# Kernel tuning notes

Measured on AMD Instinct MI355X. Metric: run time of the kernel, lower is better.

Reference implementation:

```python
import jax, jax.numpy as jnp
import numpy as np
from jax import lax

WIN = 7            # skimage default win_size
K1, K2 = 0.01, 0.03
DATA_RANGE = 1.0


def _uniform_filter_valid(x):
    # (skimage uses reflect-padded uniform_filter then crops pad=3, which equals
    #  a valid windowed mean.)
    c, h, w = x.shape
    x4 = x[:, None]                                   # (C,1,H,W)
    kh = jnp.full((1, 1, WIN, 1), 1.0 / WIN, x.dtype)
    kw = jnp.full((1, 1, 1, WIN), 1.0 / WIN, x.dtype)
    dn = ('NCHW', 'OIHW', 'NCHW')
    x4 = lax.conv_general_dilated(x4, kh, (1, 1), 'VALID', dimension_numbers=dn)
    x4 = lax.conv_general_dilated(x4, kw, (1, 1), 'VALID', dimension_numbers=dn)
    return x4[:, 0]


def setup_inputs() -> dict:
    key = jax.random.key(0)
    k1, k2 = jax.random.split(key)
    shape = (32, 3, 512, 512)
    return {
        'input_tensor': jax.random.uniform(k1, shape, dtype=jnp.float32),
        'target': jax.random.uniform(k2, shape, dtype=jnp.float32),
    }


def reference(input_tensor, target):
    h, w = input_tensor.shape[-2:]
    x = input_tensor.reshape(-1, h, w).astype(jnp.float32)
    y = target.reshape(-1, h, w).astype(jnp.float32)

    C1 = (K1 * DATA_RANGE) ** 2
    C2 = (K2 * DATA_RANGE) ** 2
    NP = WIN * WIN
    cov_norm = NP / (NP - 1.0)  # sample covariance (skimage default)

    ux = _uniform_filter_valid(x)
    uy = _uniform_filter_valid(y)
    uxx = _uniform_filter_valid(x * x)
    uyy = _uniform_filter_valid(y * y)
    uxy = _uniform_filter_valid(x * y)

    vx = cov_norm * (uxx - ux * ux)
    vy = cov_norm * (uyy - uy * uy)
    vxy = cov_norm * (uxy - ux * uy)

    S = ((2.0 * ux * uy + C1) * (2.0 * vxy + C2)) / (
        (ux * ux + uy * uy + C1) * (vx + vy + C2))
    # mean over cropped spatial map per channel, then over channels == global mean
    return jnp.mean(S)
```

## Files before the change

### kernel.cpp

```cpp
#include <hip/hip_runtime.h>


namespace {
constexpr int W       = 512;
constexpr int HH      = 512;
constexpr int NIMG    = 96;
constexpr int OW      = 506;
constexpr int RSTRIP  = 11;
constexpr int NSTRIP  = 46;
constexpr int WAVES   = NIMG * NSTRIP;
constexpr int BLOCKS  = WAVES / 4;
constexpr int NXCD    = 8;
constexpr int CPX     = BLOCKS / NXCD;
constexpr float C1s   = 0.2401f;
constexpr float C2s   = 2.1609f;
constexpr float COVN  = 49.0f / 48.0f;
constexpr double NPIX = 96.0 * 506.0 * 506.0;
}

__device__ __forceinline__ void load8(const float* __restrict__ p, float (&v)[8])
{
    float4 a = *(const float4*)(p);
    float4 b = *(const float4*)(p + 4);
    v[0] = a.x; v[1] = a.y; v[2] = a.z; v[3] = a.w;
    v[4] = b.x; v[5] = b.y; v[6] = b.z; v[7] = b.w;
}

__device__ __forceinline__ void vadd(float (&V)[5][8], const float (&x)[8], const float (&y)[8])
{
#pragma unroll
    for (int k = 0; k < 8; k++) {
        V[0][k] += x[k];
        V[1][k] += y[k];
        V[2][k] = fmaf(x[k], x[k], V[2][k]);
        V[3][k] = fmaf(y[k], y[k], V[3][k]);
        V[4][k] = fmaf(x[k], y[k], V[4][k]);
    }
}

__device__ __forceinline__ void vsub(float (&V)[5][8], const float (&x)[8], const float (&y)[8])
{
#pragma unroll
    for (int k = 0; k < 8; k++) {
        V[0][k] -= x[k];
        V[1][k] -= y[k];
        V[2][k] = fmaf(-x[k], x[k], V[2][k]);
        V[3][k] = fmaf(-y[k], y[k], V[3][k]);
        V[4][k] = fmaf(-x[k], y[k], V[4][k]);
    }
}

__device__ __forceinline__ void hssim(const float (&V)[5][8], float& sacc, int c0)
{
    float Hh[5][8];
#pragma unroll
    for (int q = 0; q < 5; q++) {
        float P[8];
        P[0] = V[q][0];
#pragma unroll
        for (int k = 1; k < 8; k++) P[k] = P[k - 1] + V[q][k];
        const float Pn0 = __shfl_down(P[0], 1);
        const float Pn1 = __shfl_down(P[1], 1);
        const float Pn2 = __shfl_down(P[2], 1);
        const float Pn3 = __shfl_down(P[3], 1);
        const float Pn4 = __shfl_down(P[4], 1);
        const float Pn5 = __shfl_down(P[5], 1);
        const float T = P[7];
        Hh[q][0] = P[6];
        Hh[q][1] = T - P[0];
        Hh[q][2] = (T - P[1]) + Pn0;
        Hh[q][3] = (T - P[2]) + Pn1;
        Hh[q][4] = (T - P[3]) + Pn2;
        Hh[q][5] = (T - P[4]) + Pn3;
        Hh[q][6] = (T - P[5]) + Pn4;
        Hh[q][7] = (T - P[6]) + Pn5;
    }

#pragma unroll
    for (int k = 0; k < 8; k++) {
        float A = Hh[0][k], B = Hh[1][k];
        float Pq = Hh[2][k], Qq = Hh[3][k], R = Hh[4][k];
        float AB  = A * B;
        float a1  = fmaf(2.0f, AB, C1s);
        float ab2 = fmaf(A, A, B * B);
        float b1  = ab2 + C1s;
        float tt  = fmaf(49.0f, R, -AB);
        float a2  = fmaf(2.0f * COVN, tt, C2s);
        float pq  = Pq + Qq;
        float t2  = fmaf(49.0f, pq, -ab2);
        float b2  = fmaf(COVN, t2, C2s);
        float num = a1 * a2;
        float den = b1 * b2;
        float r   = __builtin_amdgcn_rcpf(den);
        r = r * fmaf(-den, r, 2.0f);
        float S = num * r;
        if (c0 + k < OW) sacc += S;
    }
}

template<bool PREB, bool PRET>
__device__ __forceinline__ void ssim_row(int jj, int r0,
        const float* __restrict__ xb, const float* __restrict__ yb,
        float (&V)[5][8],
        float (&Bx)[8], float (&By)[8],
        float (&Tx)[8], float (&Ty)[8],
        float& sacc, int c0)
{
    vadd(V, Bx, By);
    if (PREB) {
        int rb = r0 + jj + 8; if (rb > HH - 1) rb = HH - 1;
        load8(xb + (size_t)rb * W, Bx);
        load8(yb + (size_t)rb * W, By);
        __builtin_amdgcn_sched_barrier(0);
    }
    hssim(V, sacc, c0);
    vsub(V, Tx, Ty);
    if (PRET) {
        int rt = r0 + jj + 2; if (rt > HH - 1) rt = HH - 1;
        load8(xb + (size_t)rt * W, Tx);
        load8(yb + (size_t)rt * W, Ty);
        __builtin_amdgcn_sched_barrier(0);
    }
}

__global__ __launch_bounds__(256, 2) void ssim_main(const float* __restrict__ X,
                                                    const float* __restrict__ Y,
                                                    double* __restrict__ partial)
{
    __shared__ float wsum[4];

    const int t    = threadIdx.x;
    const int lane = t & 63;
    const int wid  = t >> 6;

    const int bid  = blockIdx.x;
    const int swz  = (bid % NXCD) * CPX + bid / NXCD;

    const int gw    = swz * 4 + wid;
    const int img   = gw / NSTRIP;
    const int strip = gw - img * NSTRIP;
    const int r0    = strip * RSTRIP;
    const int c0    = lane * 8;

    const float* xb = X + (size_t)img * (W * HH) + c0;
    const float* yb = Y + (size_t)img * (W * HH) + c0;

    float B0x[8], B0y[8], B1x[8], B1y[8];
    float T0x[8], T0y[8], T1x[8], T1y[8];

    load8(xb + (size_t)(r0 + 6) * W, B0x); load8(yb + (size_t)(r0 + 6) * W, B0y);
    load8(xb + (size_t)(r0 + 7) * W, B1x); load8(yb + (size_t)(r0 + 7) * W, B1y);
    load8(xb + (size_t)(r0 + 0) * W, T0x); load8(yb + (size_t)(r0 + 0) * W, T0y);
    load8(xb + (size_t)(r0 + 1) * W, T1x); load8(yb + (size_t)(r0 + 1) * W, T1y);

    float V[5][8];
#pragma unroll
    for (int q = 0; q < 5; q++)
#pragma unroll
        for (int k = 0; k < 8; k++) V[q][k] = 0.0f;

    {
        float wax[8], way[8], wbx[8], wby[8];
        load8(xb + (size_t)(r0 + 2) * W, wax); load8(yb + (size_t)(r0 + 2) * W, way);
        load8(xb + (size_t)(r0 + 3) * W, wbx); load8(yb + (size_t)(r0 + 3) * W, wby);
        vadd(V, T0x, T0y);
        vadd(V, T1x, T1y);
        vadd(V, wax, way);
        load8(xb + (size_t)(r0 + 4) * W, wax); load8(yb + (size_t)(r0 + 4) * W, way);
        vadd(V, wbx, wby);
        load8(xb + (size_t)(r0 + 5) * W, wbx); load8(yb + (size_t)(r0 + 5) * W, wby);
        vadd(V, wax, way);
        vadd(V, wbx, wby);
    }

    float sacc = 0.0f;

#pragma unroll 1
    for (int j = 0; j < 8; j += 2) {
        ssim_row<true,  true >(j,     r0, xb, yb, V, B0x, B0y, T0x, T0y, sacc, c0);
        ssim_row<true,  true >(j + 1, r0, xb, yb, V, B1x, B1y, T1x, T1y, sacc, c0);
    }
    ssim_row<true,  true >( 8, r0, xb, yb, V, B0x, B0y, T0x, T0y, sacc, c0);
    ssim_row<false, false>( 9, r0, xb, yb, V, B1x, B1y, T1x, T1y, sacc, c0);
    ssim_row<false, false>(10, r0, xb, yb, V, B0x, B0y, T0x, T0y, sacc, c0);

#pragma unroll
    for (int off = 32; off > 0; off >>= 1)
        sacc += __shfl_down(sacc, off);
    if (lane == 0) wsum[wid] = sacc;
    __syncthreads();
    if (t == 0)
        partial[blockIdx.x] = (double)((wsum[0] + wsum[1]) + (wsum[2] + wsum[3]));
}

__global__ void ssim_finalize(const double* __restrict__ partial, float* __restrict__ out)
{
    __shared__ double ws[4];
    const int t = threadIdx.x;
    double s = 0.0;
    for (int i = t; i < BLOCKS; i += 256) s += partial[i];
#pragma unroll
    for (int off = 32; off > 0; off >>= 1)
        s += __shfl_down(s, off);
    if ((t & 63) == 0) ws[t >> 6] = s;
    __syncthreads();
    if (t == 0) out[0] = (float)(((ws[0] + ws[1]) + (ws[2] + ws[3])) / NPIX);
}

extern "C" void kernel_launch(void* const* d_in, const int* in_sizes, int n_in,
                              void* d_out, int out_size, void* d_ws, size_t ws_size,
                              hipStream_t stream)
{
    const float* X = (const float*)d_in[0];
    const float* Y = (const float*)d_in[1];
    float* out = (float*)d_out;
    double* partial = (double*)d_ws;

    ssim_main<<<dim3(BLOCKS), 256, 0, stream>>>(X, Y, partial);
    ssim_finalize<<<1, 256, 0, stream>>>(partial, out);
}
```

Measured before the change: 236.4 us.

## Use 8-row register ring buffer, taller strips, and one-wave blocks

Doubles the rows per strip from 11 to 22, halving the redundant 6-row halo loads per strip. It replaces the two-slot top and bottom prefetch buffers with an 8-row register ring buffer, so each loaded row is reused for both the add and the later subtract instead of being loaded twice. It also launches one 64-thread wave per block, which removes the shared-memory reduction and __syncthreads. In exchange, register pressure rises (128 floats of ring buffer), wave count halves to 2208, and the deeper prefetch is no longer guarded by sched_barrier.

```diff
diff --git a/kernel.cpp b/kernel.cpp
--- a/kernel.cpp
+++ b/kernel.cpp
@@ -6,12 +6,11 @@
 constexpr int HH      = 512;
 constexpr int NIMG    = 96;
 constexpr int OW      = 506;
-constexpr int RSTRIP  = 11;
-constexpr int NSTRIP  = 46;
+constexpr int RSTRIP  = 22;
+constexpr int NSTRIP  = 23;
 constexpr int WAVES   = NIMG * NSTRIP;
-constexpr int BLOCKS  = WAVES / 4;
 constexpr int NXCD    = 8;
-constexpr int CPX     = BLOCKS / NXCD;
+constexpr int CPX     = WAVES / NXCD;
 constexpr float C1s   = 0.2401f;
 constexpr float C2s   = 2.1609f;
 constexpr float COVN  = 49.0f / 48.0f;
@@ -98,45 +97,30 @@
     }
 }
 
-template<bool PREB, bool PRET>
-__device__ __forceinline__ void ssim_row(int jj, int r0,
+template<int SADD, int SSUB, bool PRE>
+__device__ __forceinline__ void body(int j, int r0,
         const float* __restrict__ xb, const float* __restrict__ yb,
-        float (&V)[5][8],
-        float (&Bx)[8], float (&By)[8],
-        float (&Tx)[8], float (&Ty)[8],
-        float& sacc, int c0)
-{
-    vadd(V, Bx, By);
-    if (PREB) {
-        int rb = r0 + jj + 8; if (rb > HH - 1) rb = HH - 1;
-        load8(xb + (size_t)rb * W, Bx);
-        load8(yb + (size_t)rb * W, By);
-        __builtin_amdgcn_sched_barrier(0);
-    }
+        float (&rx)[8][8], float (&ry)[8][8],
+        float (&V)[5][8], float& sacc, int c0)
+{
+    vadd(V, rx[SADD], ry[SADD]);
     hssim(V, sacc, c0);
-    vsub(V, Tx, Ty);
-    if (PRET) {
-        int rt = r0 + jj + 2; if (rt > HH - 1) rt = HH - 1;
-        load8(xb + (size_t)rt * W, Tx);
-        load8(yb + (size_t)rt * W, Ty);
-        __builtin_amdgcn_sched_barrier(0);
-    }
-}
-
-__global__ __launch_bounds__(256, 2) void ssim_main(const float* __restrict__ X,
-                                                    const float* __restrict__ Y,
-                                                    double* __restrict__ partial)
-{
-    __shared__ float wsum[4];
-
-    const int t    = threadIdx.x;
-    const int lane = t & 63;
-    const int wid  = t >> 6;
-
-    const int bid  = blockIdx.x;
-    const int swz  = (bid % NXCD) * CPX + bid / NXCD;
-
-    const int gw    = swz * 4 + wid;
+    vsub(V, rx[SSUB], ry[SSUB]);
+    if (PRE) {
+        load8(xb + (size_t)(r0 + j + 8) * W, rx[SSUB]);
+        load8(yb + (size_t)(r0 + j + 8) * W, ry[SSUB]);
+    }
+}
+
+__global__ __launch_bounds__(64, 2) void ssim_main(const float* __restrict__ X,
+                                                   const float* __restrict__ Y,
+                                                   double* __restrict__ partial)
+{
+    const int lane = threadIdx.x & 63;
+
+    const int bid = blockIdx.x;
+    const int gw  = (bid % NXCD) * CPX + bid / NXCD;
+
     const int img   = gw / NSTRIP;
     const int strip = gw - img * NSTRIP;
     const int r0    = strip * RSTRIP;
@@ -145,13 +129,13 @@
     const float* xb = X + (size_t)img * (W * HH) + c0;
     const float* yb = Y + (size_t)img * (W * HH) + c0;
 
-    float B0x[8], B0y[8], B1x[8], B1y[8];
-    float T0x[8], T0y[8], T1x[8], T1y[8];
-
-    load8(xb + (size_t)(r0 + 6) * W, B0x); load8(yb + (size_t)(r0 + 6) * W, B0y);
-    load8(xb + (size_t)(r0 + 7) * W, B1x); load8(yb + (size_t)(r0 + 7) * W, B1y);
-    load8(xb + (size_t)(r0 + 0) * W, T0x); load8(yb + (size_t)(r0 + 0) * W, T0y);
-    load8(xb + (size_t)(r0 + 1) * W, T1x); load8(yb + (size_t)(r0 + 1) * W, T1y);
+    float rx[8][8], ry[8][8];
+
+#pragma unroll
+    for (int r = 0; r < 8; r++) {
+        load8(xb + (size_t)(r0 + r) * W, rx[r]);
+        load8(yb + (size_t)(r0 + r) * W, ry[r]);
+    }
 
     float V[5][8];
 #pragma unroll
@@ -159,38 +143,33 @@
 #pragma unroll
         for (int k = 0; k < 8; k++) V[q][k] = 0.0f;
 
-    {
-        float wax[8], way[8], wbx[8], wby[8];
-        load8(xb + (size_t)(r0 + 2) * W, wax); load8(yb + (size_t)(r0 + 2) * W, way);
-        load8(xb + (size_t)(r0 + 3) * W, wbx); load8(yb + (size_t)(r0 + 3) * W, wby);
-        vadd(V, T0x, T0y);
-        vadd(V, T1x, T1y);
-        vadd(V, wax, way);
-        load8(xb + (size_t)(r0 + 4) * W, wax); load8(yb + (size_t)(r0 + 4) * W, way);
-        vadd(V, wbx, wby);
-        load8(xb + (size_t)(r0 + 5) * W, wbx); load8(yb + (size_t)(r0 + 5) * W, wby);
-        vadd(V, wax, way);
-        vadd(V, wbx, wby);
-    }
+#pragma unroll
+    for (int r = 0; r < 6; r++) vadd(V, rx[r], ry[r]);
 
     float sacc = 0.0f;
 
 #pragma unroll 1
-    for (int j = 0; j < 8; j += 2) {
-        ssim_row<true,  true >(j,     r0, xb, yb, V, B0x, B0y, T0x, T0y, sacc, c0);
-        ssim_row<true,  true >(j + 1, r0, xb, yb, V, B1x, B1y, T1x, T1y, sacc, c0);
-    }
-    ssim_row<true,  true >( 8, r0, xb, yb, V, B0x, B0y, T0x, T0y, sacc, c0);
-    ssim_row<false, false>( 9, r0, xb, yb, V, B1x, B1y, T1x, T1y, sacc, c0);
-    ssim_row<false, false>(10, r0, xb, yb, V, B0x, B0y, T0x, T0y, sacc, c0);
+    for (int jb = 0; jb < 16; jb += 8) {
+        body<6, 0, true>(jb + 0, r0, xb, yb, rx, ry, V, sacc, c0);
+        body<7, 1, true>(jb + 1, r0, xb, yb, rx, ry, V, sacc, c0);
+        body<0, 2, true>(jb + 2, r0, xb, yb, rx, ry, V, sacc, c0);
+        body<1, 3, true>(jb + 3, r0, xb, yb, rx, ry, V, sacc, c0);
+        body<2, 4, true>(jb + 4, r0, xb, yb, rx, ry, V, sacc, c0);
+        body<3, 5, true>(jb + 5, r0, xb, yb, rx, ry, V, sacc, c0);
+        body<4, 6, true>(jb + 6, r0, xb, yb, rx, ry, V, sacc, c0);
+        body<5, 7, true>(jb + 7, r0, xb, yb, rx, ry, V, sacc, c0);
+    }
+    body<6, 0, true >(16, r0, xb, yb, rx, ry, V, sacc, c0);
+    body<7, 1, true >(17, r0, xb, yb, rx, ry, V, sacc, c0);
+    body<0, 2, true >(18, r0, xb, yb, rx, ry, V, sacc, c0);
+    body<1, 3, true >(19, r0, xb, yb, rx, ry, V, sacc, c0);
+    body<2, 4, false>(20, r0, xb, yb, rx, ry, V, sacc, c0);
+    body<3, 5, false>(21, r0, xb, yb, rx, ry, V, sacc, c0);
 
 #pragma unroll
     for (int off = 32; off > 0; off >>= 1)
         sacc += __shfl_down(sacc, off);
-    if (lane == 0) wsum[wid] = sacc;
-    __syncthreads();
-    if (t == 0)
-        partial[blockIdx.x] = (double)((wsum[0] + wsum[1]) + (wsum[2] + wsum[3]));
+    if (lane == 0) partial[bid] = (double)sacc;
 }
 
 __global__ void ssim_finalize(const double* __restrict__ partial, float* __restrict__ out)
@@ -198,7 +177,7 @@
     __shared__ double ws[4];
     const int t = threadIdx.x;
     double s = 0.0;
-    for (int i = t; i < BLOCKS; i += 256) s += partial[i];
+    for (int i = t; i < WAVES; i += 256) s += partial[i];
 #pragma unroll
     for (int off = 32; off > 0; off >>= 1)
         s += __shfl_down(s, off);
@@ -216,6 +195,6 @@
     float* out = (float*)d_out;
     double* partial = (double*)d_ws;
 
-    ssim_main<<<dim3(BLOCKS), 256, 0, stream>>>(X, Y, partial);
+    ssim_main<<<dim3(WAVES), 64, 0, stream>>>(X, Y, partial);
     ssim_finalize<<<1, 256, 0, stream>>>(partial, out);
 }
```

Result: slower. 282.6 us (+19.5%).

## Split each lane's columns into two float4 halves for coalesced row loads

Applied to the files above, without the earlier changes.

Each lane now owns columns lane*4..+3 and 256+lane*4..+3 instead of eight contiguous columns, so each float4 load across the wave touches one contiguous 1KB segment. Horizontal window sums now use shuffles at distances 1 and 2, plus a wraparound from lane 0 for the seam between the two halves. The row pipeline becomes a simple rolling loop with a one-row prefetch of the incoming and outgoing rows, replacing the two-deep unrolled prefetch with sched barriers. This adds shuffle work and may expose more load latency because prefetch depth is shallower.

```diff
diff --git a/kernel.cpp b/kernel.cpp
--- a/kernel.cpp
+++ b/kernel.cpp
@@ -18,108 +18,121 @@
 constexpr double NPIX = 96.0 * 506.0 * 506.0;
 }
 
-__device__ __forceinline__ void load8(const float* __restrict__ p, float (&v)[8])
+__device__ __forceinline__ void loadrow(const float* __restrict__ p, float (&v)[2][4])
 {
     float4 a = *(const float4*)(p);
-    float4 b = *(const float4*)(p + 4);
-    v[0] = a.x; v[1] = a.y; v[2] = a.z; v[3] = a.w;
-    v[4] = b.x; v[5] = b.y; v[6] = b.z; v[7] = b.w;
-}
-
-__device__ __forceinline__ void vadd(float (&V)[5][8], const float (&x)[8], const float (&y)[8])
-{
-#pragma unroll
-    for (int k = 0; k < 8; k++) {
-        V[0][k] += x[k];
-        V[1][k] += y[k];
-        V[2][k] = fmaf(x[k], x[k], V[2][k]);
-        V[3][k] = fmaf(y[k], y[k], V[3][k]);
-        V[4][k] = fmaf(x[k], y[k], V[4][k]);
-    }
-}
-
-__device__ __forceinline__ void vsub(float (&V)[5][8], const float (&x)[8], const float (&y)[8])
-{
-#pragma unroll
-    for (int k = 0; k < 8; k++) {
-        V[0][k] -= x[k];
-        V[1][k] -= y[k];
-        V[2][k] = fmaf(-x[k], x[k], V[2][k]);
-        V[3][k] = fmaf(-y[k], y[k], V[3][k]);
-        V[4][k] = fmaf(-x[k], y[k], V[4][k]);
-    }
-}
-
-__device__ __forceinline__ void hssim(const float (&V)[5][8], float& sacc, int c0)
-{
-    float Hh[5][8];
+    float4 b = *(const float4*)(p + 256);
+    v[0][0] = a.x; v[0][1] = a.y; v[0][2] = a.z; v[0][3] = a.w;
+    v[1][0] = b.x; v[1][1] = b.y; v[1][2] = b.z; v[1][3] = b.w;
+}
+
+__device__ __forceinline__ void vadd(float (&V)[5][2][4], const float (&x)[2][4], const float (&y)[2][4])
+{
+#pragma unroll
+    for (int p = 0; p < 2; p++)
+#pragma unroll
+        for (int k = 0; k < 4; k++) {
+            V[0][p][k] += x[p][k];
+            V[1][p][k] += y[p][k];
+            V[2][p][k] = fmaf(x[p][k], x[p][k], V[2][p][k]);
+            V[3][p][k] = fmaf(y[p][k], y[p][k], V[3][p][k]);
+            V[4][p][k] = fmaf(x[p][k], y[p][k], V[4][p][k]);
+        }
+}
+
+__device__ __forceinline__ void vsub(float (&V)[5][2][4], const float (&x)[2][4], const float (&y)[2][4])
+{
+#pragma unroll
+    for (int p = 0; p < 2; p++)
+#pragma unroll
+        for (int k = 0; k < 4; k++) {
+            V[0][p][k] -= x[p][k];
+            V[1][p][k] -= y[p][k];
+            V[2][p][k] = fmaf(-x[p][k], x[p][k], V[2][p][k]);
+            V[3][p][k] = fmaf(-y[p][k], y[p][k], V[3][p][k]);
+            V[4][p][k] = fmaf(-x[p][k], y[p][k], V[4][p][k]);
+        }
+}
+
+__device__ __forceinline__ void hssim(const float (&V)[5][2][4], float& sacc, int lane)
+{
+    float HA[5][4], HB[5][4];
 #pragma unroll
     for (int q = 0; q < 5; q++) {
-        float P[8];
-        P[0] = V[q][0];
-#pragma unroll
-        for (int k = 1; k < 8; k++) P[k] = P[k - 1] + V[q][k];
-        const float Pn0 = __shfl_down(P[0], 1);
-        const float Pn1 = __shfl_down(P[1], 1);
-        const float Pn2 = __shfl_down(P[2], 1);
-        const float Pn3 = __shfl_down(P[3], 1);
-        const float Pn4 = __shfl_down(P[4], 1);
-        const float Pn5 = __shfl_down(P[5], 1);
-        const float T = P[7];
-        Hh[q][0] = P[6];
-        Hh[q][1] = T - P[0];
-        Hh[q][2] = (T - P[1]) + Pn0;
-        Hh[q][3] = (T - P[2]) + Pn1;
-        Hh[q][4] = (T - P[3]) + Pn2;
-        Hh[q][5] = (T - P[4]) + Pn3;
-        Hh[q][6] = (T - P[5]) + Pn4;
-        Hh[q][7] = (T - P[6]) + Pn5;
-    }
-
-#pragma unroll
-    for (int k = 0; k < 8; k++) {
-        float A = Hh[0][k], B = Hh[1][k];
-        float Pq = Hh[2][k], Qq = Hh[3][k], R = Hh[4][k];
-        float AB  = A * B;
-        float a1  = fmaf(2.0f, AB, C1s);
-        float ab2 = fmaf(A, A, B * B);
-        float b1  = ab2 + C1s;
-        float tt  = fmaf(49.0f, R, -AB);
-        float a2  = fmaf(2.0f * COVN, tt, C2s);
-        float pq  = Pq + Qq;
-        float t2  = fmaf(49.0f, pq, -ab2);
-        float b2  = fmaf(COVN, t2, C2s);
-        float num = a1 * a2;
-        float den = b1 * b2;
-        float r   = __builtin_amdgcn_rcpf(den);
-        r = r * fmaf(-den, r, 2.0f);
-        float S = num * r;
-        if (c0 + k < OW) sacc += S;
-    }
-}
-
-template<bool PREB, bool PRET>
-__device__ __forceinline__ void ssim_row(int jj, int r0,
-        const float* __restrict__ xb, const float* __restrict__ yb,
-        float (&V)[5][8],
-        float (&Bx)[8], float (&By)[8],
-        float (&Tx)[8], float (&Ty)[8],
-        float& sacc, int c0)
-{
-    vadd(V, Bx, By);
-    if (PREB) {
-        int rb = r0 + jj + 8; if (rb > HH - 1) rb = HH - 1;
-        load8(xb + (size_t)rb * W, Bx);
-        load8(yb + (size_t)rb * W, By);
-        __builtin_amdgcn_sched_barrier(0);
-    }
-    hssim(V, sacc, c0);
-    vsub(V, Tx, Ty);
-    if (PRET) {
-        int rt = r0 + jj + 2; if (rt > HH - 1) rt = HH - 1;
-        load8(xb + (size_t)rt * W, Tx);
-        load8(yb + (size_t)rt * W, Ty);
-        __builtin_amdgcn_sched_barrier(0);
+        const float a0 = V[q][0][0];
+        const float a1 = a0 + V[q][0][1];
+        const float a2 = a1 + V[q][0][2];
+        const float a3 = a2 + V[q][0][3];
+        const float b0 = V[q][1][0];
+        const float b1 = b0 + V[q][1][1];
+        const float b2 = b1 + V[q][1][2];
+        const float b3 = b2 + V[q][1][3];
+
+        float n1P2 = __shfl_down(a2, 1);
+        float n1P3 = __shfl_down(a3, 1);
+        float n2P0 = __shfl_down(a0, 2);
+        float n2P1 = __shfl_down(a1, 2);
+        float m1P2 = __shfl_down(b2, 1);
+        float m1P3 = __shfl_down(b3, 1);
+        float m2P0 = __shfl_down(b0, 2);
+        float m2P1 = __shfl_down(b1, 2);
+
+        const float sb00 = __shfl(b0, 0), sb10 = __shfl(b1, 0);
+        const float sb20 = __shfl(b2, 0), sb30 = __shfl(b3, 0);
+        const float sb01 = __shfl(b0, 1), sb11 = __shfl(b1, 1);
+        if (lane == 62) { n2P0 = sb00; n2P1 = sb10; }
+        if (lane == 63) { n1P2 = sb20; n1P3 = sb30; n2P0 = sb01; n2P1 = sb11; }
+
+        HA[q][0] = a3 + n1P2;
+        HA[q][1] = (a3 - a0) + n1P3;
+        HA[q][2] = (a3 - a1) + (n1P3 + n2P0);
+        HA[q][3] = (a3 - a2) + (n1P3 + n2P1);
+        HB[q][0] = b3 + m1P2;
+        HB[q][1] = (b3 - b0) + m1P3;
+        HB[q][2] = (b3 - b1) + (m1P3 + m2P0);
+        HB[q][3] = (b3 - b2) + (m1P3 + m2P1);
+    }
+
+    const int lk = lane * 4;
+#pragma unroll
+    for (int k = 0; k < 4; k++) {
+        {
+            float A = HA[0][k], B = HA[1][k];
+            float Pq = HA[2][k], Qq = HA[3][k], R = HA[4][k];
+            float AB  = A * B;
+            float a1  = fmaf(2.0f, AB, C1s);
+            float ab2 = fmaf(A, A, B * B);
+            float b1  = ab2 + C1s;
+            float tt  = fmaf(49.0f, R, -AB);
+            float a2  = fmaf(2.0f * COVN, tt, C2s);
+            float pq  = Pq + Qq;
+            float t2  = fmaf(49.0f, pq, -ab2);
+            float b2  = fmaf(COVN, t2, C2s);
+            float num = a1 * a2;
+            float den = b1 * b2;
+            float r   = __builtin_amdgcn_rcpf(den);
+            r = r * fmaf(-den, r, 2.0f);
+            sacc += num * r;
+        }
+        {
+            float A = HB[0][k], B = HB[1][k];
+            float Pq = HB[2][k], Qq = HB[3][k], R = HB[4][k];
+            float AB  = A * B;
+            float a1  = fmaf(2.0f, AB, C1s);
+            float ab2 = fmaf(A, A, B * B);
+            float b1  = ab2 + C1s;
+            float tt  = fmaf(49.0f, R, -AB);
+            float a2  = fmaf(2.0f * COVN, tt, C2s);
+            float pq  = Pq + Qq;
+            float t2  = fmaf(49.0f, pq, -ab2);
+            float b2  = fmaf(COVN, t2, C2s);
+            float num = a1 * a2;
+            float den = b1 * b2;
+            float r   = __builtin_amdgcn_rcpf(den);
+            r = r * fmaf(-den, r, 2.0f);
+            float S = num * r;
+            if (lk + k <= 249) sacc += S;
+        }
     }
 }
 
@@ -140,49 +153,63 @@
     const int img   = gw / NSTRIP;
     const int strip = gw - img * NSTRIP;
     const int r0    = strip * RSTRIP;
-    const int c0    = lane * 8;
-
-    const float* xb = X + (size_t)img * (W * HH) + c0;
-    const float* yb = Y + (size_t)img * (W * HH) + c0;
-
-    float B0x[8], B0y[8], B1x[8], B1y[8];
-    float T0x[8], T0y[8], T1x[8], T1y[8];
-
-    load8(xb + (size_t)(r0 + 6) * W, B0x); load8(yb + (size_t)(r0 + 6) * W, B0y);
-    load8(xb + (size_t)(r0 + 7) * W, B1x); load8(yb + (size_t)(r0 + 7) * W, B1y);
-    load8(xb + (size_t)(r0 + 0) * W, T0x); load8(yb + (size_t)(r0 + 0) * W, T0y);
-    load8(xb + (size_t)(r0 + 1) * W, T1x); load8(yb + (size_t)(r0 + 1) * W, T1y);
-
-    float V[5][8];
+
+    const float* xb = X + (size_t)img * (W * HH) + lane * 4;
+    const float* yb = Y + (size_t)img * (W * HH) + lane * 4;
+
+    float V[5][2][4];
 #pragma unroll
     for (int q = 0; q < 5; q++)
 #pragma unroll
-        for (int k = 0; k < 8; k++) V[q][k] = 0.0f;
-
-    {
-        float wax[8], way[8], wbx[8], wby[8];
-        load8(xb + (size_t)(r0 + 2) * W, wax); load8(yb + (size_t)(r0 + 2) * W, way);
-        load8(xb + (size_t)(r0 + 3) * W, wbx); load8(yb + (size_t)(r0 + 3) * W, wby);
-        vadd(V, T0x, T0y);
-        vadd(V, T1x, T1y);
-        vadd(V, wax, way);
-        load8(xb + (size_t)(r0 + 4) * W, wax); load8(yb + (size_t)(r0 + 4) * W, way);
-        vadd(V, wbx, wby);
-        load8(xb + (size_t)(r0 + 5) * W, wbx); load8(yb + (size_t)(r0 + 5) * W, wby);
-        vadd(V, wax, way);
-        vadd(V, wbx, wby);
-    }
+        for (int p = 0; p < 2; p++)
+#pragma unroll
+            for (int k = 0; k < 4; k++) V[q][p][k] = 0.0f;
+
+    float xo[2][4], yo[2][4];
+
+#pragma unroll
+    for (int r = 0; r < 6; r++) {
+        float xs[2][4], ys[2][4];
+        loadrow(xb + (size_t)(r0 + r) * W, xs);
+        loadrow(yb + (size_t)(r0 + r) * W, ys);
+        vadd(V, xs, ys);
+        if (r == 0) {
+#pragma unroll
+            for (int p = 0; p < 2; p++)
+#pragma unroll
+                for (int k = 0; k < 4; k++) { xo[p][k] = xs[p][k]; yo[p][k] = ys[p][k]; }
+        }
+    }
+
+    float xn[2][4], yn[2][4];
+    loadrow(xb + (size_t)(r0 + 6) * W, xn);
+    loadrow(yb + (size_t)(r0 + 6) * W, yn);
 
     float sacc = 0.0f;
 
 #pragma unroll 1
-    for (int j = 0; j < 8; j += 2) {
-        ssim_row<true,  true >(j,     r0, xb, yb, V, B0x, B0y, T0x, T0y, sacc, c0);
-        ssim_row<true,  true >(j + 1, r0, xb, yb, V, B1x, B1y, T1x, T1y, sacc, c0);
-    }
-    ssim_row<true,  true >( 8, r0, xb, yb, V, B0x, B0y, T0x, T0y, sacc, c0);
-    ssim_row<false, false>( 9, r0, xb, yb, V, B1x, B1y, T1x, T1y, sacc, c0);
-    ssim_row<false, false>(10, r0, xb, yb, V, B0x, B0y, T0x, T0y, sacc, c0);
+    for (int j = 0; j < RSTRIP; j++) {
+        vadd(V, xn, yn);
+
+        float xnp[2][4], ynp[2][4], xop[2][4], yop[2][4];
+        int rb = r0 + j + 7; if (rb > HH - 1) rb = HH - 1;
+        loadrow(xb + (size_t)rb * W, xnp);
+        loadrow(yb + (size_t)rb * W, ynp);
+        loadrow(xb + (size_t)(r0 + j + 1) * W, xop);
+        loadrow(yb + (size_t)(r0 + j + 1) * W, yop);
+
+        hssim(V, sacc, lane);
+
+        vsub(V, xo, yo);
+
+#pragma unroll
+        for (int p = 0; p < 2; p++)
+#pragma unroll
+            for (int k = 0; k < 4; k++) {
+                xn[p][k] = xnp[p][k]; yn[p][k] = ynp[p][k];
+                xo[p][k] = xop[p][k]; yo[p][k] = yop[p][k];
+            }
+    }
 
 #pragma unroll
     for (int off = 32; off > 0; off >>= 1)
```

Result: slower. 252.8 us (+6.9%).
